# Kernel optimization log

Hardware: AMD Instinct MI355X
Metric: run time of the kernel (lower is better)

Reference implementation:

```python
import jax, jax.numpy as jnp
import numpy as np

N = 10000      # nodes
E = 64000      # edges (includes N self-loops)
IN = 1247      # in_size (text 0:600, audio 600:942, video 942:)
H = 4          # num_heads
D0 = 256       # gcv[1]
D1 = 8         # gcv[2]
OUT = 6        # out_size


def setup_inputs() -> dict:
    key = jax.random.key(0)
    ks = jax.random.split(key, 24)
    s = 0.05
    feats = jax.random.normal(ks[0], (N, IN), jnp.float32)
    drop = jax.random.bernoulli(ks[1], 0.2, (N, IN))
    feats = jnp.where(drop, 0.0, feats)
    # random edges plus self-loops so every node has in-degree >= 1
    src = jnp.concatenate([jax.random.randint(ks[2], (E - N,), 0, N), jnp.arange(N)]).astype(jnp.int32)
    dst = jnp.concatenate([jax.random.randint(ks[3], (E - N,), 0, N), jnp.arange(N)]).astype(jnp.int32)
    textMask = (jnp.zeros(IN).at[:600].set(1.0) * 3.0).astype(jnp.float32)
    audioMask = (jnp.zeros(IN).at[600:942].set(1.0) * 2.0).astype(jnp.float32)
    videoMask = (jnp.zeros(IN).at[942:].set(1.0) * 1.0).astype(jnp.float32)
    return {
        'features': feats, 'src': src, 'dst': dst,
        'textMask': textMask, 'audioMask': audioMask, 'videoMask': videoMask,
        'W2': jax.random.normal(ks[4], (H, IN, D1), jnp.float32) * s,
        'a2': jax.random.normal(ks[5], (H, 2 * D1), jnp.float32) * s,
        'Wl0': jax.random.normal(ks[6], (IN, H * D0), jnp.float32) * s,
        'Wr0': jax.random.normal(ks[7], (IN, H * D0), jnp.float32) * s,
        'a0': jax.random.normal(ks[8], (H, D0), jnp.float32) * s,
        'Wres0': jax.random.normal(ks[9], (IN, H * D0), jnp.float32) * s,
        'b0': jnp.zeros((H * D0,), jnp.float32),
        'Wl1': jax.random.normal(ks[10], (H * D0, H * D1), jnp.float32) * s,
        'Wr1': jax.random.normal(ks[11], (H * D0, H * D1), jnp.float32) * s,
        'a1': jax.random.normal(ks[12], (H, D1), jnp.float32) * s,
        'Wres1': jax.random.normal(ks[13], (H * D0, H * D1), jnp.float32) * s,
        'b1': jnp.zeros((H * D1,), jnp.float32),
        'Wlin': jax.random.normal(ks[14], (2 * H * D1, OUT), jnp.float32) * s,
        'blin': jnp.zeros((OUT,), jnp.float32),
    }


def _segment_softmax(logits, seg, num):
    # logits: [E, H]; softmax over edges sharing the same destination node
    m = jax.ops.segment_max(logits, seg, num_segments=num)
    m = jnp.where(jnp.isfinite(m), m, 0.0)  # guard empty segments
    p = jnp.exp(logits - m[seg])
    denom = jax.ops.segment_sum(p, seg, num_segments=num)
    return p / jnp.maximum(denom[seg], 1e-9)


def _gatv2(x, src, dst, Wl, Wr, attn, Wres, b, h, d, n):
    # DGL GATv2Conv: e = a . leaky_relu(W_l x_u + W_r x_v), edge-softmax over dst,
    # aggregate W_l x_u, add residual projection + bias, relu activation.
    fs = (x @ Wl).reshape(n, h, d)
    fd = (x @ Wr).reshape(n, h, d)
    e = jax.nn.leaky_relu(fs[src] + fd[dst], 0.2)          # [E,H,D]
    logits = jnp.einsum('ehd,hd->eh', e, attn)             # [E,H]
    alpha = _segment_softmax(logits, dst, n)
    out = jax.ops.segment_sum(fs[src] * alpha[..., None], dst, num_segments=n)  # [N,H,D]
    out = out + (x @ Wres).reshape(n, h, d) + b.reshape(h, d)
    return jax.nn.relu(out)


def _gat_inner(x, src, dst, W, a, n):
    # classic multi-head GAT layer (concat merge): e = leaky_relu(a . [z_u || z_v])
    z = jnp.einsum('ni,hio->nho', x, W)                    # [N,H,D1]
    d = z.shape[-1]
    es = jnp.einsum('nho,ho->nh', z, a[:, :d])
    ed = jnp.einsum('nho,ho->nh', z, a[:, d:])
    logits = jax.nn.leaky_relu(es[src] + ed[dst], 0.2)     # [E,H]
    alpha = _segment_softmax(logits, dst, n)
    out = jax.ops.segment_sum(z[src] * alpha[..., None], dst, num_segments=n)
    return out.reshape(n, -1)                              # [N, H*D1]


def reference(features, src, dst, textMask, audioMask, videoMask, W2, a2,
              Wl0, Wr0, a0, Wres0, b0, Wl1, Wr1, a1, Wres1, b1, Wlin, blin):
    h = features
    # mean-impute missing (zero) entries, blend 50/50 with original
    mean = jnp.mean(h, axis=0)
    h1 = jnp.where(h == 0.0, mean[None, :], h)
    h = 0.5 * (h + h1)
    # F.normalize(p=1) per row
    h = h / jnp.maximum(jnp.sum(jnp.abs(h), axis=1, keepdims=True), 1e-12)
    # maskFilter: f*tm + f*am + f*vm
    h = h * (textMask + audioMask + videoMask)
    h3 = _gat_inner(h, src, dst, W2, a2, N)                # [N, 32]
    h = _gatv2(h, src, dst, Wl0, Wr0, a0, Wres0, b0, H, D0, N).reshape(N, -1)
    h = _gatv2(h, src, dst, Wl1, Wr1, a1, Wres1, b1, H, D1, N).reshape(N, -1)
    return jnp.concatenate([h3, h], axis=1) @ Wlin + blin  # [N, OUT]
```

## Files before the change

### kernel.cpp

```cpp
#include <hip/hip_runtime.h>
#include <hip/hip_bf16.h>

#define N_NODES 10000
#define N_EDGES 64000
#define IN_F    1247
#define KPAD    1280
#define NH      4
#define D0      256
#define D1      8
#define HD0     1024
#define HD1     32
#define NBIG    3072
#define NBIG2   3200
#define OUTF    6
#define INV_N   (1.0f / 10000.0f)
#define MPAD    10240

typedef __attribute__((ext_vector_type(8))) short bf16x8;
typedef __attribute__((ext_vector_type(4))) float f32x4;
typedef unsigned int u32;

__device__ __forceinline__ void async_copy16(const unsigned short* gsrc,
                                             unsigned short* ldst) {
    __builtin_amdgcn_global_load_lds(
        (const __attribute__((address_space(1))) u32*)(gsrc),
        (__attribute__((address_space(3))) u32*)(ldst), 16, 0, 0);
}

constexpr size_t OFF_FLAG   = 0;
constexpr size_t OFF_COLSUM = 16;
constexpr size_t OFF_MASKM  = 1296;
constexpr size_t OFF_Z      = 2576;
constexpr size_t OFF_H3     = OFF_Z    + 320000;
constexpr size_t OFF_OUT0   = OFF_H3   + 320000;
constexpr size_t OFF_FS1    = OFF_OUT0 + 10240000;
constexpr size_t OFF_FD1    = OFF_FS1  + 320000;
constexpr size_t OFF_OUT1   = OFF_FD1  + 320000;
constexpr size_t OFF_B0F    = OFF_OUT1 + 320000;
constexpr size_t OFF_B1F    = OFF_B0F  + 1024;
constexpr size_t OFF_DEG    = OFF_B1F  + 64;
constexpr size_t OFF_ROWPTR = OFF_DEG  + 10016;
constexpr size_t OFF_CURSOR = OFF_ROWPTR + 10016;
constexpr size_t OFF_CSRE   = OFF_CURSOR + 10016;
constexpr size_t OFF_FS0B   = OFF_CSRE + 64000;
constexpr size_t OFF_FD0B   = OFF_FS0B + 5120000;
constexpr size_t OFF_ABF    = OFF_FD0B + 5120000;
constexpr size_t OFF_BT     = OFF_ABF  + 6553600;
constexpr size_t OFF_BT1    = OFF_BT   + 2048000;
constexpr size_t WS_FLOATS  = OFF_BT1  + 49152;

__device__ __forceinline__ float ldin(const void* p, size_t i, int f32) {
    return f32 ? ((const float*)p)[i]
               : __bfloat162float(((const __hip_bfloat16*)p)[i]);
}
__device__ __forceinline__ float bfu2f(unsigned short u) {
    union { unsigned int i; float f; } x;
    x.i = ((unsigned int)u) << 16;
    return x.f;
}
__device__ __forceinline__ unsigned short f2bu(float v) {
    __hip_bfloat16 h = __float2bfloat16(v);
    unsigned short u;
    __builtin_memcpy(&u, &h, 2);
    return u;
}


__global__ void init_kernel(const unsigned short* __restrict__ feats_w,
                            int* __restrict__ flag, int* __restrict__ deg,
                            u32* __restrict__ btpad) {
    int b = blockIdx.x, t = threadIdx.x;
    if (b < 64) {
        int found = 0;
        for (int i = b * 256 + t; i < 131072; i += 64 * 256)
            if (((feats_w[i] >> 7) & 0xFF) == 0xFF) found = 1;
        if (found) atomicOr(flag, 1);
    } else if (b < 104) {
        int idx = (b - 64) * 256 + t;
        if (idx < N_NODES + 16) deg[idx] = 0;
    } else {
        int idx = (b - 104) * 256 + t;
        if (idx < 61440) btpad[idx] = 0;
    }
}

__global__ void prepA_kernel(const void* __restrict__ feats, const int* __restrict__ dst,
                             const void* __restrict__ tm, const void* __restrict__ am,
                             const void* __restrict__ vm, const void* __restrict__ b0,
                             const void* __restrict__ b1,
                             float* __restrict__ colsum, int* __restrict__ deg,
                             float* __restrict__ maskmul, float* __restrict__ b0f,
                             float* __restrict__ b1f, const int* __restrict__ dflag) {
    int b = blockIdx.x, t = threadIdx.x;
    if (b < 500) {
        int f32 = *dflag;
        int c = (b % 5) * 256 + t;
        if (c >= IN_F) return;
        int r0 = (b / 5) * 100;
        float s = 0.f;
        for (int r = r0; r < r0 + 100; ++r)
            s += ldin(feats, (size_t)r * IN_F + c, f32);
        atomicAdd(&colsum[c], s);
    } else if (b < 750) {
        int e = (b - 500) * 256 + t;
        if (e < N_EDGES) atomicAdd(&deg[dst[e]], 1);
    } else {
        int f32 = *dflag;
        int c = (b - 750) * 256 + t;
        if (c < IN_F) maskmul[c] = ldin(tm, c, f32) + ldin(am, c, f32) + ldin(vm, c, f32);
        if (c < HD0) b0f[c] = ldin(b0, c, f32);
        if (c < HD1) b1f[c] = ldin(b1, c, f32);
    }
}

__global__ __launch_bounds__(256) void scan_kernel(const int* __restrict__ deg,
                                                   int* __restrict__ rowptr,
                                                   int* __restrict__ cursor) {
    __shared__ int wtot[4];
    int t = threadIdx.x;
    int lane = t & 63, w = t >> 6;
    int base = t * 40;
    int s = 0;
    for (int i = 0; i < 40; ++i) {
        int idx = base + i;
        if (idx < N_NODES) s += deg[idx];
    }
    int inc = s;
#pragma unroll
    for (int d = 1; d < 64; d <<= 1) {
        int v = __shfl_up(inc, d);
        if (lane >= d) inc += v;
    }
    if (lane == 63) wtot[w] = inc;
    __syncthreads();
    int woff = 0;
    for (int ww = 0; ww < w; ++ww) woff += wtot[ww];
    int run = woff + inc - s;
    for (int i = 0; i < 40; ++i) {
        int idx = base + i;
        if (idx < N_NODES) {
            rowptr[idx] = run; cursor[idx] = run;
            run += deg[idx];
        }
    }
    if (t == 255) rowptr[N_NODES] = woff + inc;
}

__global__ void scatter_kernel(const int* __restrict__ dst, int* __restrict__ cursor,
                               int* __restrict__ csr_eid) {
    int e = blockIdx.x * 256 + threadIdx.x;
    if (e >= N_EDGES) return;
    int pos = atomicAdd(&cursor[dst[e]], 1);
    csr_eid[pos] = e;
}

__global__ __launch_bounds__(256) void prepB_kernel(
        const void* __restrict__ feats, const float* __restrict__ colsum,
        const float* __restrict__ maskmul, __hip_bfloat16* __restrict__ abf,
        const void* __restrict__ Wl0, const void* __restrict__ Wr0,
        const void* __restrict__ Wres0, const void* __restrict__ W2,
        __hip_bfloat16* __restrict__ bt,
        const void* __restrict__ Wl1, const void* __restrict__ Wr1,
        const void* __restrict__ Wres1, __hip_bfloat16* __restrict__ bt1,
        const int* __restrict__ dflag) {
    __shared__ float smem[1056];
    int b = blockIdx.x, t = threadIdx.x;
    int f32 = *dflag;
    if (b < 2560) {
        int w = t >> 6, lane = t & 63;
        int n = b * 4 + w;
        unsigned short* arow = (unsigned short*)abf + (size_t)n * KPAD;
        if (n >= N_NODES) {
#pragma unroll
            for (int j = 0; j < 20; ++j) arow[j * 64 + lane] = 0;
            return;
        }
        float v[20];
        float s = 0.f;
#pragma unroll
        for (int j = 0; j < 20; ++j) {
            int c = j * 64 + lane;
            float f = (c < IN_F) ? ldin(feats, (size_t)n * IN_F + c, f32) : 0.f;
            float vv = (f != 0.0f) ? f
                     : ((c < IN_F) ? 0.5f * colsum[c] * INV_N : 0.f);
            v[j] = vv;
            s += fabsf(vv);
        }
#pragma unroll
        for (int off = 32; off > 0; off >>= 1) s += __shfl_xor(s, off);
        float scale = 1.0f / fmaxf(s, 1e-12f);
#pragma unroll
        for (int j = 0; j < 20; ++j) {
            int c = j * 64 + lane;
            float vv = (c < IN_F) ? v[j] * scale * maskmul[c] : 0.f;
            arow[c] = f2bu(vv);
        }
    } else if (b < 2560 + 3840) {
        int b2 = b - 2560;
        int bz = b2 / 1280, rem = b2 - bz * 1280;
        int by = rem >> 5, bx = rem & 31;
        float (*tile)[33] = (float(*)[33])smem;
        int n0 = bx * 32, k0 = by * 32;
        const void* W = (bz == 0) ? Wl0 : (bz == 1) ? Wr0 : Wres0;
        int tx = t & 31, ty = t >> 5;
        for (int i = ty; i < 32; i += 8) {
            int k = k0 + i;
            tile[i][tx] = (k < IN_F) ? ldin(W, (size_t)k * HD0 + n0 + tx, f32) : 0.f;
        }
        __syncthreads();
        for (int i = ty; i < 32; i += 8)
            bt[(size_t)(bz * 1024 + n0 + i) * KPAD + k0 + tx] = __float2bfloat16(tile[tx][i]);
    } else if (b < 2560 + 3840 + 160) {
        int idx = (b - (2560 + 3840)) * 256 + t;
        if (idx >= 32 * KPAD) return;
        int n = idx / KPAD, k = idx % KPAD;
        int hh = n >> 3, o = n & 7;
        float v = (k < IN_F) ? ldin(W2, ((size_t)hh * IN_F + k) * D1 + o, f32) : 0.f;
        bt[(size_t)(NBIG + n) * KPAD + k] = __float2bfloat16(v);
    } else {
        int idx = (b - (2560 + 4000)) * 256 + t;
        if (idx >= 96 * HD0) return;
        int n = idx >> 10, k = idx & 1023;
        int seg = n >> 5, col = n & 31;
        const void* W = (seg == 0) ? Wl1 : (seg == 1) ? Wr1 : Wres1;
        bt1[idx] = __float2bfloat16(ldin(W, (size_t)k * HD1 + col, f32));
    }
}

__global__ __launch_bounds__(512) void mfma_gemm(
        const unsigned short* __restrict__ A, const unsigned short* __restrict__ BT,
        const float* __restrict__ b0f, __hip_bfloat16* __restrict__ fs0b,
        __hip_bfloat16* __restrict__ fd0b, __hip_bfloat16* __restrict__ out0r,
        float* __restrict__ z) {
    __shared__ unsigned short As0[8192], Bs0[8192];
    __shared__ unsigned short As1[8192], Bs1[8192];
    __shared__ unsigned short As2[8192], Bs2[8192];
    const int g = blockIdx.x;
    const int xcd = g & 7, jloc = g >> 3;
    const int nrep = (jloc == 0) ? 2 : 1;
    const int tid = threadIdx.x;
    const int wave = tid >> 6, lane = tid & 63;
    const int quad = lane >> 4, l16 = lane & 15;
    const int wr = wave >> 2, wc = wave & 3;
    const int wm = wr * 128, wn = wc * 64;
    const int srow = lane & 15;
    const int skc  = (lane >> 4) * 8;

#define BARX() do { __builtin_amdgcn_s_barrier();                            \
                    __builtin_amdgcn_sched_barrier(0); } while (0)

#define STAGE_A2(kt, dst) do {                                               \
        _Pragma("unroll")                                                    \
        for (int tt = 0; tt < 2; ++tt) {                                     \
            int gg = wave + 8 * tt;                                          \
            async_copy16(A + (size_t)(bm + gg * 16 + srow) * KPAD            \
                             + (kt) + skc,                                   \
                         (dst) + gg * 512);                                  \
        } } while (0)

#define STAGE_B2(kt, dst) do {                                               \
        _Pragma("unroll")                                                    \
        for (int tt = 0; tt < 2; ++tt) {                                     \
            int gg = wave + 8 * tt;                                          \
            int rr = bn + gg * 16 + srow;                                    \
            rr = rr < NBIG2 ? rr : (NBIG2 - 1);                              \
            async_copy16(BT + (size_t)rr * KPAD + (kt) + skc,                \
                         (dst) + gg * 512);                                  \
        } } while (0)

#define LOADAF(buf) do {                                                     \
        _Pragma("unroll")                                                    \
        for (int fb = 0; fb < 8; ++fb)                                       \
            af[fb] = *(const bf16x8*)((buf) + (wr * 8 + fb) * 512            \
                                      + lane * 8);                           \
    } while (0)

#define LOADBF(buf, half) do {                                               \
        _Pragma("unroll")                                                    \
        for (int jj = 0; jj < 2; ++jj)                                       \
            bfr[jj] = *(const bf16x8*)((buf) + (wc * 4 + (half) * 2 + jj)    \
                                       * 512 + lane * 8);                    \
    } while (0)

#define MFMA16(jb) do {                                                      \
        __builtin_amdgcn_s_setprio(1);                                       \
        _Pragma("unroll")                                                    \
        for (int fb = 0; fb < 8; ++fb) {                                     \
            acc[fb][(jb)]     = __builtin_amdgcn_mfma_f32_16x16x32_bf16(     \
                af[fb], bfr[0], acc[fb][(jb)], 0, 0, 0);                     \
            acc[fb][(jb) + 1] = __builtin_amdgcn_mfma_f32_16x16x32_bf16(     \
                af[fb], bfr[1], acc[fb][(jb) + 1], 0, 0, 0);                 \
        }                                                                    \
        __builtin_amdgcn_s_setprio(0);                                       \
    } while (0)

#define KSTEP(curA, curB, preA, preB, kt, dostage, endcnt) do {              \
        bf16x8 af[8], bfr[2];                                                \
        LOADAF(curA);                                                        \
        LOADBF(curB, 0);                                                     \
        if (dostage) STAGE_A2((kt), preA);                                   \
        BARX();                                                              \
        MFMA16(0);                                                           \
        BARX();                                                              \
        LOADBF(curB, 1);                                                     \
        if (dostage) STAGE_B2((kt), preB);                                   \
        BARX();                                                              \
        MFMA16(2);                                                           \
        asm volatile("s_waitcnt vmcnt(" #endcnt ")" ::: "memory");           \
        BARX();                                                              \
    } while (0)

    for (int rep = 0; rep < nrep; ++rep) {
        const int l = (rep == 0) ? jloc : 64;
        const int colt = l / 5, rowi = l - colt * 5;
        const int bm = (xcd * 5 + rowi) * 256;
        const int bn = colt * 256;

        f32x4 acc[8][4];
#pragma unroll
        for (int i = 0; i < 8; ++i)
#pragma unroll
            for (int j = 0; j < 4; ++j) acc[i][j] = (f32x4){0.f, 0.f, 0.f, 0.f};

        STAGE_A2(0, As0);  STAGE_B2(0, Bs0);
        STAGE_A2(32, As1); STAGE_B2(32, Bs1);
        asm volatile("s_waitcnt vmcnt(4)" ::: "memory");
        BARX();

        for (int m = 0; m < 36; m += 3) {
            KSTEP(As0, Bs0, As2, Bs2, (m + 2) * 32, 1, 4);
            KSTEP(As1, Bs1, As0, Bs0, (m + 3) * 32, 1, 4);
            KSTEP(As2, Bs2, As1, Bs1, (m + 4) * 32, 1, 4);
        }
        KSTEP(As0, Bs0, As2, Bs2, 38 * 32, 1, 4);
        KSTEP(As1, Bs1, As0, Bs0, 39 * 32, 1, 4);
        KSTEP(As2, Bs2, As0, Bs0, 0,       0, 0);
        KSTEP(As0, Bs0, As1, Bs1, 0,       0, 0);

        const int seg = bn >> 10;
#pragma unroll
        for (int i = 0; i < 8; ++i) {
#pragma unroll
            for (int r = 0; r < 4; ++r) {
                int gm = bm + wm + i * 16 + quad * 4 + r;
                if (gm >= N_NODES) continue;
#pragma unroll
                for (int j = 0; j < 4; ++j) {
                    int gnl = (bn & 1023) + wn + j * 16 + l16;
                    float v = acc[i][j][r];
                    if (seg == 0)      fs0b[(size_t)gm * HD0 + gnl] = __float2bfloat16(v);
                    else if (seg == 1) fd0b[(size_t)gm * HD0 + gnl] = __float2bfloat16(v);
                    else if (seg == 2) out0r[(size_t)gm * HD0 + gnl] = __float2bfloat16(v + b0f[gnl]);
                    else if (gnl < HD1) z[(size_t)gm * HD1 + gnl] = v;
                }
            }
        }
    }
#undef KSTEP
#undef MFMA16
#undef LOADBF
#undef LOADAF
#undef STAGE_B2
#undef STAGE_A2
#undef BARX
}

__global__ __launch_bounds__(256) void att0z_kernel(
        const int* __restrict__ rowptr, const int* __restrict__ csre,
        const int* __restrict__ src, const __hip_bfloat16* __restrict__ fs,
        const __hip_bfloat16* __restrict__ fd, const void* __restrict__ a0,
        const __hip_bfloat16* __restrict__ out0res, __hip_bfloat16* __restrict__ out0b,
        const float* __restrict__ z, const void* __restrict__ a2,
        float* __restrict__ h3, const int* __restrict__ dflag) {
    int f32 = *dflag;
    if (blockIdx.x >= N_NODES) {
        int n = (blockIdx.x - N_NODES) * 8 + (threadIdx.x >> 5);
        int lane = threadIdx.x & 31;
        int h = lane >> 3, o = lane & 7;
        float a2e = ldin(a2, h * 2 * D1 + o, f32);
        float a2d = ldin(a2, h * 2 * D1 + D1 + o, f32);
        float zn = z[(size_t)n * HD1 + lane];
        float edn = zn * a2d;
        edn += __shfl_xor(edn, 1); edn += __shfl_xor(edn, 2); edn += __shfl_xor(edn, 4);
        float den = 0.f, acc = 0.f;
        int start = rowptr[n], end = rowptr[n + 1];
        for (int i = start; i < end; ++i) {
            int s = src[csre[i]];
            float zs = z[(size_t)s * HD1 + lane];
            float esv = zs * a2e;
            esv += __shfl_xor(esv, 1); esv += __shfl_xor(esv, 2); esv += __shfl_xor(esv, 4);
            float x = esv + edn;
            x = x > 0.f ? x : 0.2f * x;
            float p = expf(x);
            den += p;
            acc += p * zs;
        }
        h3[(size_t)n * HD1 + lane] = acc / fmaxf(den, 1e-9f);
        return;
    }
    int n = blockIdx.x;
    int t = threadIdx.x;
    __shared__ float sfd[HD0];
    __shared__ float sa0[HD0];
    __shared__ int sidx[128];
    int start = rowptr[n], end = rowptr[n + 1];
    int deg = end - start;
    {
        const unsigned short* fdp = (const unsigned short*)fd + (size_t)n * HD0;
        ushort4 u = *(const ushort4*)(fdp + 4 * t);
        sfd[4 * t + 0] = bfu2f(u.x); sfd[4 * t + 1] = bfu2f(u.y);
        sfd[4 * t + 2] = bfu2f(u.z); sfd[4 * t + 3] = bfu2f(u.w);
#pragma unroll
        for (int i = 0; i < 4; ++i) sa0[4 * t + i] = ldin(a0, 4 * t + i, f32);
        if (t < deg && t < 128) sidx[t] = src[csre[start + t]];
    }
    __syncthreads();
    const unsigned short* fsu = (const unsigned short*)fs;
    float den = 0.f;
    float acc[4] = {0.f, 0.f, 0.f, 0.f};
#pragma unroll 2
    for (int i = 0; i < deg; ++i) {
        int s = (i < 128) ? sidx[i] : src[csre[start + i]];
        ushort4 u = *(const ushort4*)(fsu + (size_t)s * HD0 + 4 * t);
        float fv[4], part = 0.f;
#pragma unroll
        for (int j = 0; j < 4; ++j) {
            unsigned short uj = (j == 0) ? u.x : (j == 1) ? u.y : (j == 2) ? u.z : u.w;
            fv[j] = bfu2f(uj);
            float x = fv[j] + sfd[4 * t + j];
            x = x > 0.f ? x : 0.2f * x;
            part += x * sa0[4 * t + j];
        }
        for (int off = 32; off > 0; off >>= 1) part += __shfl_xor(part, off);
        float p = expf(part);
        den += p;
#pragma unroll
        for (int j = 0; j < 4; ++j) acc[j] += p * fv[j];
    }
    float inv = 1.0f / fmaxf(den, 1e-9f);
    ushort4 ub = *(const ushort4*)((const unsigned short*)out0res + (size_t)n * HD0 + 4 * t);
    ushort4 o;
    o.x = f2bu(fmaxf(bfu2f(ub.x) + acc[0] * inv, 0.f));
    o.y = f2bu(fmaxf(bfu2f(ub.y) + acc[1] * inv, 0.f));
    o.z = f2bu(fmaxf(bfu2f(ub.z) + acc[2] * inv, 0.f));
    o.w = f2bu(fmaxf(bfu2f(ub.w) + acc[3] * inv, 0.f));
    *(ushort4*)((unsigned short*)out0b + (size_t)n * HD0 + 4 * t) = o;
}

__global__ __launch_bounds__(256) void mfma_gemm96(
        const unsigned short* __restrict__ A, const unsigned short* __restrict__ BT1,
        const float* __restrict__ b1f, float* __restrict__ fs1,
        float* __restrict__ fd1, float* __restrict__ out1,
        float* __restrict__ fs1b, float* __restrict__ fd1b,
        float* __restrict__ out1b) {
    __shared__ unsigned short As0[2048], Bs0[3072], As1[2048], Bs1[3072];
    const int tid = threadIdx.x;
    const int wave = tid >> 6, lane = tid & 63;
    const int quad = lane >> 4, l16 = lane & 15;
    const int bk = blockIdx.x >= 157;
    const int bm = (blockIdx.x - (bk ? 157 : 0)) * 64;
    const int kbase = bk ? 512 : 0;
    const int srow = lane & 15;
    const int skc  = (lane >> 4) * 8;
    const int NIT = 512 / 32;

    f32x4 acc[6];
#pragma unroll
    for (int j = 0; j < 6; ++j) acc[j] = (f32x4){0.f, 0.f, 0.f, 0.f};

#define STAGE96(kk, Adst, Bdst) do {                                              \
        async_copy16(A + (size_t)(bm + wave * 16 + srow) * HD0 + kbase + (kk) + skc, \
                     (Adst) + wave * 512);                                        \
        async_copy16(BT1 + (size_t)(wave * 16 + srow) * HD0 + kbase + (kk) + skc, \
                     (Bdst) + wave * 512);                                        \
        if (wave < 2)                                                             \
            async_copy16(BT1 + (size_t)((4 + wave) * 16 + srow) * HD0 + kbase + (kk) + skc, \
                         (Bdst) + (4 + wave) * 512);                              \
        } while (0)

#define COMPUTE96(Asrc, Bsrc) do {                                                \
        bf16x8 af = *(const bf16x8*)((Asrc) + wave * 512 + lane * 8);             \
        _Pragma("unroll")                                                         \
        for (int j = 0; j < 6; ++j) {                                             \
            bf16x8 bfr = *(const bf16x8*)((Bsrc) + j * 512 + lane * 8);           \
            acc[j] = __builtin_amdgcn_mfma_f32_16x16x32_bf16(af, bfr, acc[j], 0, 0, 0); \
        } } while (0)

    STAGE96(0, As0, Bs0);
    for (int it = 0; it < NIT; it += 2) {
        asm volatile("s_waitcnt vmcnt(0)" ::: "memory");
        asm volatile("s_barrier" ::: "memory");
        STAGE96((it + 1) * 32, As1, Bs1);
        COMPUTE96(As0, Bs0);
        asm volatile("s_waitcnt vmcnt(0)" ::: "memory");
        asm volatile("s_barrier" ::: "memory");
        if (it + 2 < NIT) STAGE96((it + 2) * 32, As0, Bs0);
        COMPUTE96(As1, Bs1);
    }
#undef STAGE96
#undef COMPUTE96

#pragma unroll
    for (int r = 0; r < 4; ++r) {
        int gm = bm + wave * 16 + quad * 4 + r;
        if (gm >= N_NODES) continue;
#pragma unroll
        for (int j = 0; j < 6; ++j) {
            int col = j * 16 + l16;
            int seg = col >> 5, cl = col & 31;
            float v = acc[j][r];
            if (!bk) {
                if (seg == 0)      fs1[(size_t)gm * HD1 + cl] = v;
                else if (seg == 1) fd1[(size_t)gm * HD1 + cl] = v;
                else               out1[(size_t)gm * HD1 + cl] = v + b1f[cl];
            } else {
                if (seg == 0)      fs1b[(size_t)gm * HD1 + cl] = v;
                else if (seg == 1) fd1b[(size_t)gm * HD1 + cl] = v;
                else               out1b[(size_t)gm * HD1 + cl] = v;
            }
        }
    }
}

__global__ __launch_bounds__(256) void att32e_final_kernel(
        const int* __restrict__ rowptr, const int* __restrict__ csre,
        const int* __restrict__ src, const float* __restrict__ fs1,
        const float* __restrict__ fd1, const void* __restrict__ a1,
        const float* __restrict__ out1g, const float* __restrict__ h3,
        const void* __restrict__ Wlin, const void* __restrict__ blin,
        void* __restrict__ out, const int* __restrict__ dflag,
        const float* __restrict__ fs1b, const float* __restrict__ fd1b,
        const float* __restrict__ out1gb) {
    int f32 = *dflag;
    int n = blockIdx.x * 8 + (threadIdx.x >> 5);
    int lane = threadIdx.x & 31;
    size_t ni = (size_t)n * HD1 + lane;
    float fdn = fd1[ni] + fd1b[ni];
    float a = ldin(a1, lane, f32);
    float den = 0.f, acc = 0.f;
    int start = rowptr[n], end = rowptr[n + 1];
    for (int i = start; i < end; ++i) {
        int s = src[csre[i]];
        size_t si = (size_t)s * HD1 + lane;
        float fsv = fs1[si] + fs1b[si];
        float x = fsv + fdn;
        x = x > 0.f ? x : 0.2f * x;
        float term = x * a;
        term += __shfl_xor(term, 1);
        term += __shfl_xor(term, 2);
        term += __shfl_xor(term, 4);
        float p = expf(term);
        den += p;
        acc += p * fsv;
    }
    float out1v = fmaxf(out1g[ni] + out1gb[ni] + acc / fmaxf(den, 1e-9f), 0.f);
    float h3v = h3[ni];
    float partial[OUTF];
#pragma unroll
    for (int o = 0; o < OUTF; ++o)
        partial[o] = h3v * ldin(Wlin, (size_t)lane * OUTF + o, f32)
                   + out1v * ldin(Wlin, (size_t)(HD1 + lane) * OUTF + o, f32);
#pragma unroll
    for (int st = 1; st <= 16; st <<= 1)
#pragma unroll
        for (int o = 0; o < OUTF; ++o) partial[o] += __shfl_xor(partial[o], st);
    if (lane == 0) {
#pragma unroll
        for (int o = 0; o < OUTF; ++o) {
            float v = partial[o] + ldin(blin, o, f32);
            if (f32) ((float*)out)[(size_t)n * OUTF + o] = v;
            else     ((__hip_bfloat16*)out)[(size_t)n * OUTF + o] = __float2bfloat16(v);
        }
    }
}

extern "C" void kernel_launch(void* const* d_in, const int* in_sizes, int n_in,
                              void* d_out, int out_size, void* d_ws, size_t ws_size,
                              hipStream_t stream) {
    const void* feats = d_in[0];
    const int*  src   = (const int*)d_in[1];
    const int*  dst   = (const int*)d_in[2];
    const void* tm    = d_in[3];
    const void* am    = d_in[4];
    const void* vm    = d_in[5];
    const void* W2    = d_in[6];
    const void* a2    = d_in[7];
    const void* Wl0   = d_in[8];
    const void* Wr0   = d_in[9];
    const void* a0    = d_in[10];
    const void* Wres0 = d_in[11];
    const void* b0    = d_in[12];
    const void* Wl1   = d_in[13];
    const void* Wr1   = d_in[14];
    const void* a1    = d_in[15];
    const void* Wres1 = d_in[16];
    const void* b1    = d_in[17];
    const void* Wlin  = d_in[18];
    const void* blin  = d_in[19];

    float* ws = (float*)d_ws;
    int*   dflag  = (int*)(ws + OFF_FLAG);
    float* colsum = ws + OFF_COLSUM;
    float* maskm  = ws + OFF_MASKM;
    float* z      = ws + OFF_Z;
    float* h3     = ws + OFF_H3;
    float* fs1    = ws + OFF_FS1;
    float* fd1    = ws + OFF_FD1;
    float* out1   = ws + OFF_OUT1;
    float* b0f    = ws + OFF_B0F;
    float* b1f    = ws + OFF_B1F;
    int*   deg    = (int*)(ws + OFF_DEG);
    int*   rowptr = (int*)(ws + OFF_ROWPTR);
    int*   cursor = (int*)(ws + OFF_CURSOR);
    int*   csre   = (int*)(ws + OFF_CSRE);
    __hip_bfloat16* out0r = (__hip_bfloat16*)(ws + OFF_OUT0);
    __hip_bfloat16* fs0b = (__hip_bfloat16*)(ws + OFF_FS0B);
    __hip_bfloat16* fd0b = (__hip_bfloat16*)(ws + OFF_FD0B);
    __hip_bfloat16* abf  = (__hip_bfloat16*)(ws + OFF_ABF);
    __hip_bfloat16* bt   = (__hip_bfloat16*)(ws + OFF_BT);
    __hip_bfloat16* bt1  = (__hip_bfloat16*)(ws + OFF_BT1);
    __hip_bfloat16* out0b = fd0b;
    float* fs1b  = ws + OFF_ABF;
    float* fd1b  = ws + OFF_ABF + 320000;
    float* out1b = ws + OFF_ABF + 640000;

    (void)hipMemsetAsync(ws, 0, (16 + 1280) * sizeof(float), stream);

    init_kernel<<<344, 256, 0, stream>>>((const unsigned short*)feats, dflag, deg,
                                         (u32*)(bt + (size_t)(NBIG + HD1) * KPAD));
    prepA_kernel<<<755, 256, 0, stream>>>(feats, dst, tm, am, vm, b0, b1,
                                          colsum, deg, maskm, b0f, b1f, dflag);
    scan_kernel<<<1, 256, 0, stream>>>(deg, rowptr, cursor);
    scatter_kernel<<<(N_EDGES + 255) / 256, 256, 0, stream>>>(dst, cursor, csre);

    prepB_kernel<<<2560 + 3840 + 160 + 384, 256, 0, stream>>>(
        feats, colsum, maskm, abf, Wl0, Wr0, Wres0, W2, bt, Wl1, Wr1, Wres1, bt1, dflag);

    mfma_gemm<<<512, 512, 0, stream>>>(
        (const unsigned short*)abf, (const unsigned short*)bt, b0f, fs0b, fd0b, out0r, z);

    att0z_kernel<<<N_NODES + N_NODES / 8, 256, 0, stream>>>(
        rowptr, csre, src, fs0b, fd0b, a0, out0r, out0b, z, a2, h3, dflag);

    mfma_gemm96<<<314, 256, 0, stream>>>(
        (const unsigned short*)out0b, (const unsigned short*)bt1, b1f,
        fs1, fd1, out1, fs1b, fd1b, out1b);

    att32e_final_kernel<<<N_NODES / 8, 256, 0, stream>>>(
        rowptr, csre, src, fs1, fd1, a1, out1, h3, Wlin, blin, d_out, dflag,
        fs1b, fd1b, out1b);
}
```

Measured before the change: 492.3 us.

## Compute W2 projection in prep kernel and drop extra GEMM column tile

The 32-column W2 projection (z) is now computed inside the row-normalisation pass of prepB, using an LDS copy of each normalised row and a per-lane dot product over W2. That projection no longer rides as an extra 256-wide column tile in the bf16 MFMA GEMM, which previously forced 32 blocks to run a second pass. The GEMM grid shrinks to exactly 480 tiles, and the W2 transpose and padding-zero work are removed. The cost is heavier prepB row blocks, which now do scalar FMAs with strided W2 loads, and a larger shared-memory allocation. z is also now computed in fp32 from the normalised rows rather than through the bf16 GEMM.

```diff
diff --git a/kernel.cpp b/kernel.cpp
--- a/kernel.cpp
+++ b/kernel.cpp
@@ -11,7 +11,6 @@
 #define HD0     1024
 #define HD1     32
 #define NBIG    3072
-#define NBIG2   3200
 #define OUTF    6
 #define INV_N   (1.0f / 10000.0f)
 #define MPAD    10240
@@ -67,20 +66,16 @@
 
 
 __global__ void init_kernel(const unsigned short* __restrict__ feats_w,
-                            int* __restrict__ flag, int* __restrict__ deg,
-                            u32* __restrict__ btpad) {
+                            int* __restrict__ flag, int* __restrict__ deg) {
     int b = blockIdx.x, t = threadIdx.x;
     if (b < 64) {
         int found = 0;
         for (int i = b * 256 + t; i < 131072; i += 64 * 256)
             if (((feats_w[i] >> 7) & 0xFF) == 0xFF) found = 1;
         if (found) atomicOr(flag, 1);
-    } else if (b < 104) {
+    } else {
         int idx = (b - 64) * 256 + t;
         if (idx < N_NODES + 16) deg[idx] = 0;
-    } else {
-        int idx = (b - 104) * 256 + t;
-        if (idx < 61440) btpad[idx] = 0;
     }
 }
 
@@ -162,8 +157,8 @@
         __hip_bfloat16* __restrict__ bt,
         const void* __restrict__ Wl1, const void* __restrict__ Wr1,
         const void* __restrict__ Wres1, __hip_bfloat16* __restrict__ bt1,
-        const int* __restrict__ dflag) {
-    __shared__ float smem[1056];
+        float* __restrict__ z, const int* __restrict__ dflag) {
+    __shared__ float smem[5120];
     int b = blockIdx.x, t = threadIdx.x;
     int f32 = *dflag;
     if (b < 2560) {
@@ -175,6 +170,7 @@
             for (int j = 0; j < 20; ++j) arow[j * 64 + lane] = 0;
             return;
         }
+        float* vlds = smem + w * 1280;
         float v[20];
         float s = 0.f;
 #pragma unroll
@@ -194,7 +190,25 @@
             int c = j * 64 + lane;
             float vv = (c < IN_F) ? v[j] * scale * maskmul[c] : 0.f;
             arow[c] = f2bu(vv);
-        }
+            vlds[c] = vv;
+        }
+        int out = lane & 31, half = lane >> 5;
+        int hh = out >> 3, oo = out & 7;
+        int cbeg = half * 640;
+        int cend = half ? IN_F : 640;
+        float p0 = 0.f, p1 = 0.f, p2 = 0.f, p3 = 0.f;
+        int c = cbeg;
+        for (; c + 3 < cend; c += 4) {
+            p0 += vlds[c]     * ldin(W2, ((size_t)hh * IN_F + c)     * D1 + oo, f32);
+            p1 += vlds[c + 1] * ldin(W2, ((size_t)hh * IN_F + c + 1) * D1 + oo, f32);
+            p2 += vlds[c + 2] * ldin(W2, ((size_t)hh * IN_F + c + 2) * D1 + oo, f32);
+            p3 += vlds[c + 3] * ldin(W2, ((size_t)hh * IN_F + c + 3) * D1 + oo, f32);
+        }
+        for (; c < cend; ++c)
+            p0 += vlds[c] * ldin(W2, ((size_t)hh * IN_F + c) * D1 + oo, f32);
+        float part = (p0 + p1) + (p2 + p3);
+        part += __shfl_xor(part, 32);
+        if (lane < 32) z[(size_t)n * HD1 + out] = part;
     } else if (b < 2560 + 3840) {
         int b2 = b - 2560;
         int bz = b2 / 1280, rem = b2 - bz * 1280;
@@ -210,15 +224,8 @@
         __syncthreads();
         for (int i = ty; i < 32; i += 8)
             bt[(size_t)(bz * 1024 + n0 + i) * KPAD + k0 + tx] = __float2bfloat16(tile[tx][i]);
-    } else if (b < 2560 + 3840 + 160) {
+    } else {
         int idx = (b - (2560 + 3840)) * 256 + t;
-        if (idx >= 32 * KPAD) return;
-        int n = idx / KPAD, k = idx % KPAD;
-        int hh = n >> 3, o = n & 7;
-        float v = (k < IN_F) ? ldin(W2, ((size_t)hh * IN_F + k) * D1 + o, f32) : 0.f;
-        bt[(size_t)(NBIG + n) * KPAD + k] = __float2bfloat16(v);
-    } else {
-        int idx = (b - (2560 + 4000)) * 256 + t;
         if (idx >= 96 * HD0) return;
         int n = idx >> 10, k = idx & 1023;
         int seg = n >> 5, col = n & 31;
@@ -230,21 +237,29 @@
 __global__ __launch_bounds__(512) void mfma_gemm(
         const unsigned short* __restrict__ A, const unsigned short* __restrict__ BT,
         const float* __restrict__ b0f, __hip_bfloat16* __restrict__ fs0b,
-        __hip_bfloat16* __restrict__ fd0b, __hip_bfloat16* __restrict__ out0r,
-        float* __restrict__ z) {
+        __hip_bfloat16* __restrict__ fd0b, __hip_bfloat16* __restrict__ out0r) {
     __shared__ unsigned short As0[8192], Bs0[8192];
     __shared__ unsigned short As1[8192], Bs1[8192];
     __shared__ unsigned short As2[8192], Bs2[8192];
     const int g = blockIdx.x;
-    const int xcd = g & 7, jloc = g >> 3;
-    const int nrep = (jloc == 0) ? 2 : 1;
     const int tid = threadIdx.x;
     const int wave = tid >> 6, lane = tid & 63;
     const int quad = lane >> 4, l16 = lane & 15;
+    const int srow = lane & 15;
+    const int skc  = (lane >> 4) * 8;
+
+    const int xcd = g & 7, l = g >> 3;
+    const int colt = l / 5, rowi = l - colt * 5;
+    const int bm = (xcd * 5 + rowi) * 256;
+    const int bn = colt * 256;
     const int wr = wave >> 2, wc = wave & 3;
     const int wm = wr * 128, wn = wc * 64;
-    const int srow = lane & 15;
-    const int skc  = (lane >> 4) * 8;
+
+    f32x4 acc[8][4];
+#pragma unroll
+    for (int i = 0; i < 8; ++i)
+#pragma unroll
+        for (int j = 0; j < 4; ++j) acc[i][j] = (f32x4){0.f, 0.f, 0.f, 0.f};
 
 #define BARX() do { __builtin_amdgcn_s_barrier();                            \
                     __builtin_amdgcn_sched_barrier(0); } while (0)
@@ -262,9 +277,8 @@
         _Pragma("unroll")                                                    \
         for (int tt = 0; tt < 2; ++tt) {                                     \
             int gg = wave + 8 * tt;                                          \
-            int rr = bn + gg * 16 + srow;                                    \
-            rr = rr < NBIG2 ? rr : (NBIG2 - 1);                              \
-            async_copy16(BT + (size_t)rr * KPAD + (kt) + skc,                \
+            async_copy16(BT + (size_t)(bn + gg * 16 + srow) * KPAD           \
+                             + (kt) + skc,                                   \
                          (dst) + gg * 512);                                  \
         } } while (0)
 
@@ -310,52 +324,20 @@
         BARX();                                                              \
     } while (0)
 
-    for (int rep = 0; rep < nrep; ++rep) {
-        const int l = (rep == 0) ? jloc : 64;
-        const int colt = l / 5, rowi = l - colt * 5;
-        const int bm = (xcd * 5 + rowi) * 256;
-        const int bn = colt * 256;
-
-        f32x4 acc[8][4];
-#pragma unroll
-        for (int i = 0; i < 8; ++i)
-#pragma unroll
-            for (int j = 0; j < 4; ++j) acc[i][j] = (f32x4){0.f, 0.f, 0.f, 0.f};
-
-        STAGE_A2(0, As0);  STAGE_B2(0, Bs0);
-        STAGE_A2(32, As1); STAGE_B2(32, Bs1);
-        asm volatile("s_waitcnt vmcnt(4)" ::: "memory");
-        BARX();
-
-        for (int m = 0; m < 36; m += 3) {
-            KSTEP(As0, Bs0, As2, Bs2, (m + 2) * 32, 1, 4);
-            KSTEP(As1, Bs1, As0, Bs0, (m + 3) * 32, 1, 4);
-            KSTEP(As2, Bs2, As1, Bs1, (m + 4) * 32, 1, 4);
-        }
-        KSTEP(As0, Bs0, As2, Bs2, 38 * 32, 1, 4);
-        KSTEP(As1, Bs1, As0, Bs0, 39 * 32, 1, 4);
-        KSTEP(As2, Bs2, As0, Bs0, 0,       0, 0);
-        KSTEP(As0, Bs0, As1, Bs1, 0,       0, 0);
-
-        const int seg = bn >> 10;
-#pragma unroll
-        for (int i = 0; i < 8; ++i) {
-#pragma unroll
-            for (int r = 0; r < 4; ++r) {
-                int gm = bm + wm + i * 16 + quad * 4 + r;
-                if (gm >= N_NODES) continue;
-#pragma unroll
-                for (int j = 0; j < 4; ++j) {
-                    int gnl = (bn & 1023) + wn + j * 16 + l16;
-                    float v = acc[i][j][r];
-                    if (seg == 0)      fs0b[(size_t)gm * HD0 + gnl] = __float2bfloat16(v);
-                    else if (seg == 1) fd0b[(size_t)gm * HD0 + gnl] = __float2bfloat16(v);
-                    else if (seg == 2) out0r[(size_t)gm * HD0 + gnl] = __float2bfloat16(v + b0f[gnl]);
-                    else if (gnl < HD1) z[(size_t)gm * HD1 + gnl] = v;
-                }
-            }
-        }
-    }
+    STAGE_A2(0, As0);  STAGE_B2(0, Bs0);
+    STAGE_A2(32, As1); STAGE_B2(32, Bs1);
+    asm volatile("s_waitcnt vmcnt(4)" ::: "memory");
+    BARX();
+
+    for (int m = 0; m < 36; m += 3) {
+        KSTEP(As0, Bs0, As2, Bs2, (m + 2) * 32, 1, 4);
+        KSTEP(As1, Bs1, As0, Bs0, (m + 3) * 32, 1, 4);
+        KSTEP(As2, Bs2, As1, Bs1, (m + 4) * 32, 1, 4);
+    }
+    KSTEP(As0, Bs0, As2, Bs2, 38 * 32, 1, 4);
+    KSTEP(As1, Bs1, As0, Bs0, 39 * 32, 1, 4);
+    KSTEP(As2, Bs2, As0, Bs0, 0,       0, 0);
+    KSTEP(As0, Bs0, As1, Bs1, 0,       0, 0);
 #undef KSTEP
 #undef MFMA16
 #undef LOADBF
@@ -363,6 +345,24 @@
 #undef STAGE_B2
 #undef STAGE_A2
 #undef BARX
+
+    const int seg = bn >> 10;
+#pragma unroll
+    for (int i = 0; i < 8; ++i) {
+#pragma unroll
+        for (int r = 0; r < 4; ++r) {
+            int gm = bm + wm + i * 16 + quad * 4 + r;
+            if (gm >= N_NODES) continue;
+#pragma unroll
+            for (int j = 0; j < 4; ++j) {
+                int gnl = (bn & 1023) + wn + j * 16 + l16;
+                float v = acc[i][j][r];
+                if (seg == 0)      fs0b[(size_t)gm * HD0 + gnl] = __float2bfloat16(v);
+                else if (seg == 1) fd0b[(size_t)gm * HD0 + gnl] = __float2bfloat16(v);
+                else               out0r[(size_t)gm * HD0 + gnl] = __float2bfloat16(v + b0f[gnl]);
+            }
+        }
+    }
 }
 
 __global__ __launch_bounds__(256) void att0z_kernel(
@@ -626,18 +626,18 @@
 
     (void)hipMemsetAsync(ws, 0, (16 + 1280) * sizeof(float), stream);
 
-    init_kernel<<<344, 256, 0, stream>>>((const unsigned short*)feats, dflag, deg,
-                                         (u32*)(bt + (size_t)(NBIG + HD1) * KPAD));
+    init_kernel<<<104, 256, 0, stream>>>((const unsigned short*)feats, dflag, deg);
     prepA_kernel<<<755, 256, 0, stream>>>(feats, dst, tm, am, vm, b0, b1,
                                           colsum, deg, maskm, b0f, b1f, dflag);
     scan_kernel<<<1, 256, 0, stream>>>(deg, rowptr, cursor);
     scatter_kernel<<<(N_EDGES + 255) / 256, 256, 0, stream>>>(dst, cursor, csre);
 
-    prepB_kernel<<<2560 + 3840 + 160 + 384, 256, 0, stream>>>(
-        feats, colsum, maskm, abf, Wl0, Wr0, Wres0, W2, bt, Wl1, Wr1, Wres1, bt1, dflag);
-
-    mfma_gemm<<<512, 512, 0, stream>>>(
-        (const unsigned short*)abf, (const unsigned short*)bt, b0f, fs0b, fd0b, out0r, z);
+    prepB_kernel<<<2560 + 3840 + 384, 256, 0, stream>>>(
+        feats, colsum, maskm, abf, Wl0, Wr0, Wres0, W2, bt, Wl1, Wr1, Wres1,
+        bt1, z, dflag);
+
+    mfma_gemm<<<480, 512, 0, stream>>>(
+        (const unsigned short*)abf, (const unsigned short*)bt, b0f, fs0b, fd0b, out0r);
 
     att0z_kernel<<<N_NODES + N_NODES / 8, 256, 0, stream>>>(
         rowptr, csre, src, fs0b, fd0b, a0, out0r, out0b, z, a2, h3, dflag);
```

Result: slower. 590.7 us (+20.0%).
